# Kernel tuning notes

Measured on AMD Instinct MI355X. Metric: run time of the kernel, lower is better.

The kernel has to match this reference:

```python
import jax, jax.numpy as jnp
import numpy as np

D_MODEL = 1024
N_HEADS = 16
D_K = D_MODEL // N_HEADS
B, S = 4, 2048


def _xavier(key, out_dim, in_dim):
    limit = float(np.sqrt(6.0 / (in_dim + out_dim)))
    return jax.random.uniform(key, (out_dim, in_dim), jnp.float32, -limit, limit)


def setup_inputs() -> dict:
    key = jax.random.key(0)
    ks = jax.random.split(key, 7)
    return {
        "query": jax.random.normal(ks[0], (B, S, D_MODEL), jnp.float32),
        "key": jax.random.normal(ks[1], (B, S, D_MODEL), jnp.float32),
        "value": jax.random.normal(ks[2], (B, S, D_MODEL), jnp.float32),
        "W_q": _xavier(ks[3], D_MODEL, D_MODEL), "b_q": jnp.zeros((D_MODEL,), jnp.float32),
        "W_k": _xavier(ks[4], D_MODEL, D_MODEL), "b_k": jnp.zeros((D_MODEL,), jnp.float32),
        "W_v": _xavier(ks[5], D_MODEL, D_MODEL), "b_v": jnp.zeros((D_MODEL,), jnp.float32),
        "W_o": _xavier(ks[6], D_MODEL, D_MODEL), "b_o": jnp.zeros((D_MODEL,), jnp.float32),
    }


def reference(query, key, value, W_q, b_q, W_k, b_k, W_v, b_v, W_o, b_o):
    b, sq, _ = query.shape
    sk = key.shape[1]
    # Linear projections (torch Linear: x @ W.T + b), then split heads -> (b, h, s, d_k)
    Q = (query @ W_q.T + b_q).reshape(b, sq, N_HEADS, D_K).transpose(0, 2, 1, 3)
    K = (key @ W_k.T + b_k).reshape(b, sk, N_HEADS, D_K).transpose(0, 2, 1, 3)
    V = (value @ W_v.T + b_v).reshape(b, sk, N_HEADS, D_K).transpose(0, 2, 1, 3)
    # Naive full-score attention: (b, h, sq, sk) materialized, as in the original
    scores = jnp.einsum("bhqd,bhkd->bhqk", Q, K) / jnp.sqrt(jnp.float32(D_K))
    attn = jax.nn.softmax(scores, axis=-1)
    out = jnp.einsum("bhqk,bhkd->bhqd", attn, V)
    out = out.transpose(0, 2, 1, 3).reshape(b, sq, D_MODEL)
    return out @ W_o.T + b_o
```

## Files before the change

kernel.cpp:

```cpp
#include <hip/hip_runtime.h>
#include <hip/hip_bf16.h>
#include <cstdint>
#include <cstddef>

typedef unsigned short u16;
typedef unsigned int u32;
typedef __attribute__((ext_vector_type(8))) short bf16x8;
typedef __attribute__((ext_vector_type(4))) float f32x4;
typedef __attribute__((ext_vector_type(16))) float f32x16;
typedef __attribute__((ext_vector_type(4))) unsigned int u32x4;
typedef __attribute__((ext_vector_type(4))) unsigned short u16x4;

#define MFMA16(A,B,C) __builtin_amdgcn_mfma_f32_16x16x32_bf16(A,B,C,0,0,0)
#define MFMA32(A,B,C) __builtin_amdgcn_mfma_f32_32x32x16_bf16(A,B,C,0,0,0)

__device__ __forceinline__ u16 f2bf(float x) {
  __hip_bfloat16 h = __float2bfloat16(x);
  return __builtin_bit_cast(u16, h);
}

__device__ __forceinline__ float fast_exp2(float x) {
  float r;
  asm("v_exp_f32 %0, %1" : "=v"(r) : "v"(x));
  return r;
}

__device__ __forceinline__ void async_copy16(u16* lds, const u16* g) {
  __builtin_amdgcn_global_load_lds(
      (const __attribute__((address_space(1))) void*)g,
      (__attribute__((address_space(3))) void*)lds, 16, 0, 0);
}

__global__ void cvt4_kernel(const float* __restrict__ i0, const float* __restrict__ i1,
                            const float* __restrict__ i2, const float* __restrict__ i3,
                            u16* __restrict__ o0, u16* __restrict__ o1,
                            u16* __restrict__ o2, u16* __restrict__ o3, int n4) {
  const float* in; u16* out;
  switch (blockIdx.y) {
    case 0:  in = i0; out = o0; break;
    case 1:  in = i1; out = o1; break;
    case 2:  in = i2; out = o2; break;
    default: in = i3; out = o3; break;
  }
  int i = blockIdx.x * blockDim.x + threadIdx.x;
  int stride = gridDim.x * blockDim.x;
  for (; i < n4; i += stride) {
    float4 v = reinterpret_cast<const float4*>(in)[i];
    u16x4 o;
    o.x = f2bf(v.x); o.y = f2bf(v.y); o.z = f2bf(v.z); o.w = f2bf(v.w);
    reinterpret_cast<u16x4*>(out)[i] = o;
  }
}

template<bool BF16OUT>
__global__ __launch_bounds__(256, 2)
void gemm_nt_bias(const u16* __restrict__ A, const u16* __restrict__ W,
                  const float* __restrict__ bias, void* __restrict__ Cout,
                  int M, int N, int K, float scale) {
  __shared__ __attribute__((aligned(16))) u16 As[128*32];
  __shared__ __attribute__((aligned(16))) u16 Bs[128*32];
  const int t = threadIdx.x;
  const int lane = t & 63, wid = t >> 6;
  const int wr = wid >> 1, wc = wid & 1;
  const int g = lane >> 4, qc = lane & 15;
  const size_t m0 = (size_t)blockIdx.y * 128;
  const size_t n0 = (size_t)blockIdx.x * 128;
  f32x4 acc[4][4] = {};

  for (int k0 = 0; k0 < K; k0 += 32) {
    __syncthreads();
    #pragma unroll
    for (int c = 0; c < 2; ++c) {
      int s = c*256 + t;
      int row = s >> 2, ch = s & 3;
      int sch = ch ^ ((row >> 1) & 3);
      async_copy16(&As[s*8], &A[(m0 + row)*K + k0 + sch*8]);
    }
    #pragma unroll
    for (int c = 0; c < 2; ++c) {
      int s = c*256 + t;
      int row = s >> 2, ch = s & 3;
      int sch = ch ^ ((row >> 1) & 3);
      async_copy16(&Bs[s*8], &W[(n0 + row)*K + k0 + sch*8]);
    }
    __syncthreads();
    bf16x8 af[4], bfr[4];
    #pragma unroll
    for (int i = 0; i < 4; ++i) {
      int r = wr*64 + i*16 + qc;
      int ch = g ^ ((r >> 1) & 3);
      af[i] = *reinterpret_cast<const bf16x8*>(&As[r*32 + ch*8]);
    }
    #pragma unroll
    for (int j = 0; j < 4; ++j) {
      int r = wc*64 + j*16 + qc;
      int ch = g ^ ((r >> 1) & 3);
      bfr[j] = *reinterpret_cast<const bf16x8*>(&Bs[r*32 + ch*8]);
    }
    #pragma unroll
    for (int i = 0; i < 4; ++i)
      #pragma unroll
      for (int j = 0; j < 4; ++j)
        acc[i][j] = MFMA16(af[i], bfr[j], acc[i][j]);
  }

  #pragma unroll
  for (int j = 0; j < 4; ++j) {
    size_t col = n0 + wc*64 + j*16 + qc;
    float bv = bias[col];
    #pragma unroll
    for (int i = 0; i < 4; ++i) {
      #pragma unroll
      for (int r = 0; r < 4; ++r) {
        size_t row = m0 + wr*64 + i*16 + g*4 + r;
        float v = (acc[i][j][r] + bv) * scale;
        if (BF16OUT) ((u16*)Cout)[row*N + col] = f2bf(v);
        else         ((float*)Cout)[row*N + col] = v;
      }
    }
  }
}

__global__ __launch_bounds__(512, 4)
void flash_attn3(const u16* __restrict__ Qp, const u16* __restrict__ Kp,
                 const u16* __restrict__ Vp, u16* __restrict__ O) {
  __shared__ __attribute__((aligned(16))) u16 Ks[2][64*64];
  __shared__ __attribute__((aligned(16))) u16 Vt[3][64*64];
  const int t = threadIdx.x;
  const int w = t >> 6, lane = t & 63;
  const int l31 = lane & 31, hi = lane >> 5;
  const int bh = blockIdx.y;
  const size_t rowbase = (size_t)(bh >> 4) * 2048;
  const int hoff = (bh & 15) * 64;
  const int q0 = blockIdx.x * 256 + w * 32;
  const float THR = 11.5415603f;

  bf16x8 bq[4];
  {
    const u16* qp = &Qp[(rowbase + q0 + l31) * 1024 + hoff + hi * 8];
    #pragma unroll
    for (int dd = 0; dd < 4; ++dd) bq[dd] = *reinterpret_cast<const bf16x8*>(qp + dd*16);
  }

  f32x16 accO[2] = {};
  float m_run = 0.f, l_run = 0.f;
  u32 pwp[2][8];

  const int kvr_s = t >> 3, c_s = t & 7;
  const int sc_s = c_s ^ ((kvr_s >> 3) & 7);
  const int vd0_s = (t & 7) * 8;
  const int vcs = kvr_s >> 3;

  async_copy16(&Ks[0][t*8], &Kp[(rowbase + kvr_s)*1024 + hoff + sc_s*8]);
  bf16x8 vreg = *reinterpret_cast<const bf16x8*>(&Vp[(rowbase + kvr_s)*1024 + hoff + vd0_s]);

  int wi = 0, ri = 2;
  for (int kv = 0; kv < 32; ++kv) {
    const int kb = kv & 1;
    u16* vw = &Vt[0][0] + wi*4096;
    const u16* vrd = &Vt[0][0] + ri*4096;

    #pragma unroll
    for (int j = 0; j < 8; ++j) {
      int d = vd0_s + j;
      vw[d*64 + ((vcs ^ ((d>>3)&7))*8) + (kvr_s & 7)] = (u16)vreg[j];
    }
    __syncthreads();
    if (kv < 31) {
      const size_t nb = rowbase + (size_t)(kv+1)*64;
      async_copy16(&Ks[kb^1][t*8], &Kp[(nb + kvr_s)*1024 + hoff + sc_s*8]);
      vreg = *reinterpret_cast<const bf16x8*>(&Vp[(nb + kvr_s)*1024 + hoff + vd0_s]);
    }

    f32x16 sacc[2];
    {
      const float negm = -m_run;
      #pragma unroll
      for (int i = 0; i < 16; ++i) { sacc[0][i] = negm; sacc[1][i] = negm; }
    }
    #pragma unroll
    for (int n = 0; n < 2; ++n) {
      int kvr = n*32 + l31;
      int swz = (kvr >> 3) & 7;
      #pragma unroll
      for (int dd = 0; dd < 4; ++dd) {
        int ch = (2*dd + hi) ^ swz;
        bf16x8 ak = *reinterpret_cast<const bf16x8*>(&Ks[kb][kvr*64 + ch*8]);
        sacc[n] = MFMA32(ak, bq[dd], sacc[n]);
      }
    }

    if (kv > 0) {
      #pragma unroll
      for (int ks = 0; ks < 4; ++ks) {
        const int n = ks >> 1, kp = ks & 1;
        u32 wA0 = pwp[n][4*kp+0], wA1 = pwp[n][4*kp+1];
        u32 wB0 = pwp[n][4*kp+2], wB1 = pwp[n][4*kp+3];
        u32 s0 = hi ? wA0 : wB0, s1 = hi ? wA1 : wB1;
        u32 r0 = (u32)__shfl_xor((int)s0, 32);
        u32 r1 = (u32)__shfl_xor((int)s1, 32);
        u32 k0 = hi ? wB0 : wA0, k1 = hi ? wB1 : wA1;
        u32x4 fu;
        fu.x = hi ? r0 : k0; fu.y = hi ? r1 : k1;
        fu.z = hi ? k0 : r0; fu.w = hi ? k1 : r1;
        bf16x8 pa = __builtin_bit_cast(bf16x8, fu);
        #pragma unroll
        for (int dt = 0; dt < 2; ++dt) {
          int d = dt*32 + l31;
          int ch = (2*ks + hi) ^ ((d>>3)&7);
          bf16x8 bv = *reinterpret_cast<const bf16x8*>(&vrd[d*64 + ch*8]);
          accO[dt] = MFMA32(pa, bv, accO[dt]);
        }
      }
    }

    float a0 = fmaxf(fmaxf(sacc[0][0],sacc[0][1]),sacc[0][2]);
    float a1 = fmaxf(fmaxf(sacc[0][3],sacc[0][4]),sacc[0][5]);
    float a2 = fmaxf(fmaxf(sacc[0][6],sacc[0][7]),sacc[0][8]);
    float a3 = fmaxf(fmaxf(sacc[0][9],sacc[0][10]),sacc[0][11]);
    float a4 = fmaxf(fmaxf(sacc[0][12],sacc[0][13]),sacc[0][14]);
    float a5 = fmaxf(fmaxf(sacc[0][15],sacc[1][0]),sacc[1][1]);
    float a6 = fmaxf(fmaxf(sacc[1][2],sacc[1][3]),sacc[1][4]);
    float a7 = fmaxf(fmaxf(sacc[1][5],sacc[1][6]),sacc[1][7]);
    float a8 = fmaxf(fmaxf(sacc[1][8],sacc[1][9]),sacc[1][10]);
    float a9 = fmaxf(fmaxf(sacc[1][11],sacc[1][12]),sacc[1][13]);
    float aA = fmaxf(sacc[1][14],sacc[1][15]);
    float b0 = fmaxf(fmaxf(a0,a1),a2);
    float b1 = fmaxf(fmaxf(a3,a4),a5);
    float b2 = fmaxf(fmaxf(a6,a7),a8);
    float b3 = fmaxf(a9,aA);
    float mloc = fmaxf(fmaxf(b0,b1),fmaxf(b2,b3));
    float mx = fmaxf(mloc, __shfl_xor(mloc, 32));

    if (__any(mx > THR)) {
      float dm = fmaxf(mx, 0.f);
      float alpha = fast_exp2(-dm);
      m_run += dm;
      l_run *= alpha;
      #pragma unroll
      for (int n = 0; n < 2; ++n)
        #pragma unroll
        for (int r = 0; r < 16; ++r) sacc[n][r] -= dm;
      #pragma unroll
      for (int r = 0; r < 16; ++r) {
        int qrow = (r&3) + 8*(r>>2) + 4*hi;
        float ar = __shfl(alpha, qrow);
        accO[0][r] *= ar; accO[1][r] *= ar;
      }
    }

    #pragma unroll
    for (int n = 0; n < 2; ++n)
      #pragma unroll
      for (int r = 0; r < 16; ++r) sacc[n][r] = fast_exp2(sacc[n][r]);
    #pragma unroll
    for (int n = 0; n < 2; ++n)
      #pragma unroll
      for (int i = 0; i < 8; ++i)
        pwp[n][i] = (u32)f2bf(sacc[n][2*i]) | ((u32)f2bf(sacc[n][2*i+1]) << 16);
    float ts[16];
    #pragma unroll
    for (int i = 0; i < 16; ++i) ts[i] = sacc[0][i] + sacc[1][i];
    #pragma unroll
    for (int off = 8; off >= 1; off >>= 1)
      #pragma unroll
      for (int i = 0; i < off; ++i) ts[i] += ts[i + off];
    l_run += ts[0] + __shfl_xor(ts[0], 32);

    wi = (wi == 2) ? 0 : wi + 1;
    ri = (ri == 2) ? 0 : ri + 1;
  }

  {
    const u16* vrd = &Vt[0][0] + ri*4096;
    #pragma unroll
    for (int ks = 0; ks < 4; ++ks) {
      const int n = ks >> 1, kp = ks & 1;
      u32 wA0 = pwp[n][4*kp+0], wA1 = pwp[n][4*kp+1];
      u32 wB0 = pwp[n][4*kp+2], wB1 = pwp[n][4*kp+3];
      u32 s0 = hi ? wA0 : wB0, s1 = hi ? wA1 : wB1;
      u32 r0 = (u32)__shfl_xor((int)s0, 32);
      u32 r1 = (u32)__shfl_xor((int)s1, 32);
      u32 k0 = hi ? wB0 : wA0, k1 = hi ? wB1 : wA1;
      u32x4 fu;
      fu.x = hi ? r0 : k0; fu.y = hi ? r1 : k1;
      fu.z = hi ? k0 : r0; fu.w = hi ? k1 : r1;
      bf16x8 pa = __builtin_bit_cast(bf16x8, fu);
      #pragma unroll
      for (int dt = 0; dt < 2; ++dt) {
        int d = dt*32 + l31;
        int ch = (2*ks + hi) ^ ((d>>3)&7);
        bf16x8 bv = *reinterpret_cast<const bf16x8*>(&vrd[d*64 + ch*8]);
        accO[dt] = MFMA32(pa, bv, accO[dt]);
      }
    }
  }

  float linv = 1.0f / l_run;
  #pragma unroll
  for (int r = 0; r < 16; ++r) {
    int qrow = (r&3) + 8*(r>>2) + 4*hi;
    float lv = __shfl(linv, qrow);
    size_t orow = rowbase + q0 + qrow;
    O[orow*1024 + hoff + l31]      = f2bf(accO[0][r] * lv);
    O[orow*1024 + hoff + 32 + l31] = f2bf(accO[1][r] * lv);
  }
}

extern "C" void kernel_launch(void* const* d_in, const int* in_sizes, int n_in,
                              void* d_out, int out_size, void* d_ws, size_t ws_size,
                              hipStream_t stream) {
  (void)in_sizes; (void)n_in; (void)out_size; (void)ws_size;
  const float* query = (const float*)d_in[0];
  const float* key   = (const float*)d_in[1];
  const float* value = (const float*)d_in[2];
  const float* W_q   = (const float*)d_in[3];
  const float* b_q   = (const float*)d_in[4];
  const float* W_k   = (const float*)d_in[5];
  const float* b_k   = (const float*)d_in[6];
  const float* W_v   = (const float*)d_in[7];
  const float* b_v   = (const float*)d_in[8];
  const float* W_o   = (const float*)d_in[9];
  const float* b_o   = (const float*)d_in[10];

  const size_t sz_t = (size_t)8192 * 1024;
  const size_t sz_w = (size_t)1024 * 1024;
  u16* ws = (u16*)d_ws;
  u16* xq = ws;
  u16* xk = ws + 1*sz_t;
  u16* xv = ws + 2*sz_t;
  u16* Qp = ws + 3*sz_t;
  u16* Kp = ws + 4*sz_t;
  u16* Vp = ws + 5*sz_t;
  u16* wq = ws + 6*sz_t;
  u16* wk = wq + sz_w;
  u16* wv = wq + 2*sz_w;
  u16* wo = wq + 3*sz_w;

  const float SCL = 0.125f * 1.44269504089f;

  cvt4_kernel<<<dim3(512, 4), 256, 0, stream>>>(W_q, W_k, W_v, W_o,
                                                wq, wk, wv, wo, (int)(sz_w/4));
  cvt4_kernel<<<dim3(2048, 3), 256, 0, stream>>>(query, key, value, value,
                                                 xq, xk, xv, xv, (int)(sz_t/4));

  dim3 gg(1024/128, 8192/128);
  gemm_nt_bias<true><<<gg, 256, 0, stream>>>(xq, wq, b_q, Qp, 8192, 1024, 1024, SCL);
  gemm_nt_bias<true><<<gg, 256, 0, stream>>>(xk, wk, b_k, Kp, 8192, 1024, 1024, 1.0f);
  gemm_nt_bias<true><<<gg, 256, 0, stream>>>(xv, wv, b_v, Vp, 8192, 1024, 1024, 1.0f);

  flash_attn3<<<dim3(8, 64), 512, 0, stream>>>(Qp, Kp, Vp, xq);

  gemm_nt_bias<false><<<gg, 256, 0, stream>>>(xq, wo, b_o, d_out, 8192, 1024, 1024, 1.0f);
}
```

Before: 250.2 us.

## Use permlane32 swap, MFMA priority hints, and swap grid dims for locality

Replaces the __shfl_xor(…,32) exchanges and their select logic with v_permlane32_swap in the P-operand build and the max/sum reductions. Raises wave priority around the MFMA blocks with s_setprio. Swaps the grid x/y dimensions in the GEMMs and attention so consecutively scheduled blocks share weight tiles or K/V heads. This is meant to cut cross-lane (LDS-based) shuffle cost and improve cache reuse, at the risk of worse L2 behaviour from the new block order.

```diff
diff --git a/kernel.cpp b/kernel.cpp
--- a/kernel.cpp
+++ b/kernel.cpp
@@ -23,6 +23,10 @@
   float r;
   asm("v_exp_f32 %0, %1" : "=v"(r) : "v"(x));
   return r;
+}
+
+__device__ __forceinline__ void permswap(u32& a, u32& b) {
+  asm("v_permlane32_swap_b32 %0, %1" : "+v"(a), "+v"(b));
 }
 
 __device__ __forceinline__ void async_copy16(u16* lds, const u16* g) {
@@ -63,8 +67,8 @@
   const int lane = t & 63, wid = t >> 6;
   const int wr = wid >> 1, wc = wid & 1;
   const int g = lane >> 4, qc = lane & 15;
-  const size_t m0 = (size_t)blockIdx.y * 128;
-  const size_t n0 = (size_t)blockIdx.x * 128;
+  const size_t m0 = (size_t)blockIdx.x * 128;
+  const size_t n0 = (size_t)blockIdx.y * 128;
   f32x4 acc[4][4] = {};
 
   for (int k0 = 0; k0 < K; k0 += 32) {
@@ -129,10 +133,10 @@
   const int t = threadIdx.x;
   const int w = t >> 6, lane = t & 63;
   const int l31 = lane & 31, hi = lane >> 5;
-  const int bh = blockIdx.y;
+  const int bh = blockIdx.x;
   const size_t rowbase = (size_t)(bh >> 4) * 2048;
   const int hoff = (bh & 15) * 64;
-  const int q0 = blockIdx.x * 256 + w * 32;
+  const int q0 = blockIdx.y * 256 + w * 32;
   const float THR = 11.5415603f;
 
   bf16x8 bq[4];
@@ -178,6 +182,7 @@
       #pragma unroll
       for (int i = 0; i < 16; ++i) { sacc[0][i] = negm; sacc[1][i] = negm; }
     }
+    __builtin_amdgcn_s_setprio(1);
     #pragma unroll
     for (int n = 0; n < 2; ++n) {
       int kvr = n*32 + l31;
@@ -189,20 +194,19 @@
         sacc[n] = MFMA32(ak, bq[dd], sacc[n]);
       }
     }
+    __builtin_amdgcn_s_setprio(0);
 
     if (kv > 0) {
+      __builtin_amdgcn_s_setprio(1);
       #pragma unroll
       for (int ks = 0; ks < 4; ++ks) {
         const int n = ks >> 1, kp = ks & 1;
         u32 wA0 = pwp[n][4*kp+0], wA1 = pwp[n][4*kp+1];
         u32 wB0 = pwp[n][4*kp+2], wB1 = pwp[n][4*kp+3];
-        u32 s0 = hi ? wA0 : wB0, s1 = hi ? wA1 : wB1;
-        u32 r0 = (u32)__shfl_xor((int)s0, 32);
-        u32 r1 = (u32)__shfl_xor((int)s1, 32);
-        u32 k0 = hi ? wB0 : wA0, k1 = hi ? wB1 : wA1;
+        permswap(wA0, wB0);
+        permswap(wA1, wB1);
         u32x4 fu;
-        fu.x = hi ? r0 : k0; fu.y = hi ? r1 : k1;
-        fu.z = hi ? k0 : r0; fu.w = hi ? k1 : r1;
+        fu.x = wA0; fu.y = wA1; fu.z = wB0; fu.w = wB1;
         bf16x8 pa = __builtin_bit_cast(bf16x8, fu);
         #pragma unroll
         for (int dt = 0; dt < 2; ++dt) {
@@ -212,6 +216,7 @@
           accO[dt] = MFMA32(pa, bv, accO[dt]);
         }
       }
+      __builtin_amdgcn_s_setprio(0);
     }
 
     float a0 = fmaxf(fmaxf(sacc[0][0],sacc[0][1]),sacc[0][2]);
@@ -230,7 +235,13 @@
     float b2 = fmaxf(fmaxf(a6,a7),a8);
     float b3 = fmaxf(a9,aA);
     float mloc = fmaxf(fmaxf(b0,b1),fmaxf(b2,b3));
-    float mx = fmaxf(mloc, __shfl_xor(mloc, 32));
+    float mx;
+    {
+      u32 ma = __builtin_bit_cast(u32, mloc), mb = ma;
+      permswap(ma, mb);
+      float other = __builtin_bit_cast(float, hi ? ma : mb);
+      mx = fmaxf(mloc, other);
+    }
 
     if (__any(mx > THR)) {
       float dm = fmaxf(mx, 0.f);
@@ -265,7 +276,12 @@
     for (int off = 8; off >= 1; off >>= 1)
       #pragma unroll
       for (int i = 0; i < off; ++i) ts[i] += ts[i + off];
-    l_run += ts[0] + __shfl_xor(ts[0], 32);
+    {
+      u32 sa = __builtin_bit_cast(u32, ts[0]), sb = sa;
+      permswap(sa, sb);
+      float other = __builtin_bit_cast(float, hi ? sa : sb);
+      l_run += ts[0] + other;
+    }
 
     wi = (wi == 2) ? 0 : wi + 1;
     ri = (ri == 2) ? 0 : ri + 1;
@@ -273,18 +289,16 @@
 
   {
     const u16* vrd = &Vt[0][0] + ri*4096;
+    __builtin_amdgcn_s_setprio(1);
     #pragma unroll
     for (int ks = 0; ks < 4; ++ks) {
       const int n = ks >> 1, kp = ks & 1;
       u32 wA0 = pwp[n][4*kp+0], wA1 = pwp[n][4*kp+1];
       u32 wB0 = pwp[n][4*kp+2], wB1 = pwp[n][4*kp+3];
-      u32 s0 = hi ? wA0 : wB0, s1 = hi ? wA1 : wB1;
-      u32 r0 = (u32)__shfl_xor((int)s0, 32);
-      u32 r1 = (u32)__shfl_xor((int)s1, 32);
-      u32 k0 = hi ? wB0 : wA0, k1 = hi ? wB1 : wA1;
+      permswap(wA0, wB0);
+      permswap(wA1, wB1);
       u32x4 fu;
-      fu.x = hi ? r0 : k0; fu.y = hi ? r1 : k1;
-      fu.z = hi ? k0 : r0; fu.w = hi ? k1 : r1;
+      fu.x = wA0; fu.y = wA1; fu.z = wB0; fu.w = wB1;
       bf16x8 pa = __builtin_bit_cast(bf16x8, fu);
       #pragma unroll
       for (int dt = 0; dt < 2; ++dt) {
@@ -294,6 +308,7 @@
         accO[dt] = MFMA32(pa, bv, accO[dt]);
       }
     }
+    __builtin_amdgcn_s_setprio(0);
   }
 
   float linv = 1.0f / l_run;
@@ -344,12 +359,12 @@
   cvt4_kernel<<<dim3(2048, 3), 256, 0, stream>>>(query, key, value, value,
                                                  xq, xk, xv, xv, (int)(sz_t/4));
 
-  dim3 gg(1024/128, 8192/128);
+  dim3 gg(8192/128, 1024/128);
   gemm_nt_bias<true><<<gg, 256, 0, stream>>>(xq, wq, b_q, Qp, 8192, 1024, 1024, SCL);
   gemm_nt_bias<true><<<gg, 256, 0, stream>>>(xk, wk, b_k, Kp, 8192, 1024, 1024, 1.0f);
   gemm_nt_bias<true><<<gg, 256, 0, stream>>>(xv, wv, b_v, Vp, 8192, 1024, 1024, 1.0f);
 
-  flash_attn3<<<dim3(8, 64), 512, 0, stream>>>(Qp, Kp, Vp, xq);
+  flash_attn3<<<dim3(64, 8), 512, 0, stream>>>(Qp, Kp, Vp, xq);
 
   gemm_nt_bias<false><<<gg, 256, 0, stream>>>(xq, wo, b_o, d_out, 8192, 1024, 1024, 1.0f);
 }
```

After: 242.2 us. 1.03x faster.
